# Optimization experiments

Hardware: AMD Instinct MI355X
Metric: run time of the kernel (lower is better)

Reference implementation:

```python
import jax, jax.numpy as jnp
import numpy as np

DIM = 768
CA = 192  # int(dim * mlp_ratio)
T = 8

def setup_inputs() -> dict:
    key = jax.random.key(0)
    ks = jax.random.split(key, 7)
    x = jax.random.normal(ks[0], (197, 128, DIM), dtype=jnp.float32)
    w1 = jax.random.normal(ks[1], (DIM, CA), dtype=jnp.float32) * 0.02
    b1 = jax.random.normal(ks[2], (CA,), dtype=jnp.float32) * 0.02
    conv_w = jax.random.normal(ks[3], (CA, 3), dtype=jnp.float32) * 0.02  # depthwise temporal kernel (3,1,1)
    conv_b = jax.random.normal(ks[4], (CA,), dtype=jnp.float32) * 0.02
    w2 = jax.random.normal(ks[5], (CA, DIM), dtype=jnp.float32) * 0.02
    b2 = jax.random.normal(ks[6], (DIM,), dtype=jnp.float32) * 0.02
    return {"x": x, "w1": w1, "b1": b1, "conv_w": conv_w, "conv_b": conv_b, "w2": w2, "b2": b2}

def reference(x, w1, b1, conv_w, conv_b, w2, b2):
    # x: (L, BT, dim), tokens-first layout (fc1 applied before permute)
    x_id = x
    h = x @ w1 + b1                      # (L, BT, Ca)
    h = jnp.transpose(h, (1, 0, 2))      # (BT, L, Ca)
    BT, L, Ca = h.shape
    B = BT // T
    h = h[:, 1:, :]                      # drop first token (L-1 patch tokens)
    x_cls = h[:, :1, :]                  # (BT, 1, Ca) -- first token AFTER the slice (as in original)
    x_temp = h.reshape(B, T, L - 1, Ca)  # (B, T, P, Ca)
    # Depthwise Conv3d with kernel (3,1,1), pad (1,0,0): pure temporal depthwise conv.
    xp = jnp.pad(x_temp, ((0, 0), (1, 1), (0, 0), (0, 0)))
    x_after = (xp[:, :-2] * conv_w[:, 0] + xp[:, 1:-1] * conv_w[:, 1]
               + xp[:, 2:] * conv_w[:, 2] + conv_b)  # (B, T, P, Ca)
    # Triangular-masked pairwise diff: sum_{i<j} (x_after[j] - x_temp[i]) / 28,
    # computed without materializing the (B,T,T,P,Ca) diff tensor:
    # each x_after[j] appears j times; each x_temp[i] appears (T-1-i) times.
    t = jnp.arange(T, dtype=x.dtype)
    result = (jnp.einsum('t,btpc->bpc', t, x_after)
              - jnp.einsum('t,btpc->bpc', (T - 1) - t, x_temp)) / 28.0
    x_last = (x_temp + result[:, None]).reshape(BT, L - 1, Ca)
    out = jnp.concatenate([x_cls, x_last], axis=1)   # (BT, L, Ca)
    out = jnp.transpose(out, (1, 0, 2))              # (L, BT, Ca)
    out = jax.nn.gelu(out, approximate=False)        # torch nn.GELU default = exact erf
    out = out @ w2 + b2                              # (L, BT, dim)
    return x_id + out
```

## Files before the change

kernel.cpp:

```cpp
#include <hip/hip_runtime.h>
#include <hip/hip_bf16.h>
#include <math.h>

#define DIM   768
#define CA    192
#define NTOK  25216

typedef __attribute__((ext_vector_type(8))) short short8;
typedef __attribute__((ext_vector_type(4))) float f32x4;

static __device__ __forceinline__ short f2bf(float f) {
    union { __hip_bfloat16 b; short s; } u;
    u.b = __float2bfloat16(f);
    return u.s;
}
static __device__ __forceinline__ float gelu_exact(float x) {
    return 0.5f * x * (1.0f + erff(x * 0.70710678118654752440f));
}
static __device__ __forceinline__ void ld16(void* lds, const void* gsrc) {
    __builtin_amdgcn_global_load_lds((const __attribute__((address_space(1))) void*)gsrc,
                                     (__attribute__((address_space(3))) void*)lds, 16, 0, 0);
}

__global__ void prep_kernel(const float* __restrict__ w1, const float* __restrict__ w2,
                            short* __restrict__ w1T, short* __restrict__ w2T) {
    int idx = blockIdx.x * 256 + threadIdx.x;
    if (idx < CA * DIM) {
        int n = idx / DIM, k = idx - n * DIM;
        w1T[idx] = f2bf(w1[k * CA + n]);
        int n2 = idx / CA, k2 = idx - n2 * CA;
        w2T[idx] = f2bf(w2[k2 * DIM + n2]);
    }
}

__global__ __launch_bounds__(256) void gemm1_fused(
        const float* __restrict__ x, const short* __restrict__ w1T,
        const float* __restrict__ b1, const float* __restrict__ conv_w,
        const float* __restrict__ conv_b, short* __restrict__ gq) {
    __shared__ __align__(16) short As[64 * 40];
    __shared__ __align__(16) short Bs[2][96 * 32];

    const int tid = threadIdx.x;
    const int bx  = blockIdx.x;
    const int l   = (bx >> 2) + 1;
    const int hm  = (bx >> 1) & 1;
    const int n0  = (bx & 1) * 96;
    const int R0  = l * 128 + hm * 64;

    const int wave = tid >> 6, lane = tid & 63;
    const int wm = wave >> 1, wn = wave & 1;
    const int lm = lane & 15, lg = lane >> 4;
    const int lk = lg * 8;

    const int arow = tid >> 2;
    const int acol = (tid & 3) * 8;
    const float* xrow = x + (size_t)(R0 + arow) * DIM + acol;

    f32x4 acc[2][3] = {};

    f32x4 av0 = *(const f32x4*)(xrow);
    f32x4 av1 = *(const f32x4*)(xrow + 4);
    if (wave < 3) {
        #pragma unroll
        for (int j = 0; j < 2; j++) {
            int s = (wave * 2 + j) * 64 + lane;
            int m = s >> 2;
            int q = (s & 3) ^ ((m >> 1) & 3);
            ld16(&Bs[0][(wave * 2 + j) * 512], w1T + (size_t)(n0 + m) * DIM + q * 8);
        }
    }

    for (int i = 0; i < 24; i++) {
        const int p = i & 1;
        short8 a8;
        #pragma unroll
        for (int e = 0; e < 4; e++) { a8[e] = f2bf(av0[e]); a8[4 + e] = f2bf(av1[e]); }
        __syncthreads();
        *(short8*)&As[arow * 40 + acol] = a8;
        __syncthreads();
        if (i < 23) {
            const float* xn = xrow + (i + 1) * 32;
            av0 = *(const f32x4*)(xn);
            av1 = *(const f32x4*)(xn + 4);
            if (wave < 3) {
                const int k0n = (i + 1) * 32;
                #pragma unroll
                for (int j = 0; j < 2; j++) {
                    int s = (wave * 2 + j) * 64 + lane;
                    int m = s >> 2;
                    int q = (s & 3) ^ ((m >> 1) & 3);
                    ld16(&Bs[1 - p][(wave * 2 + j) * 512],
                         w1T + (size_t)(n0 + m) * DIM + k0n + q * 8);
                }
            }
        }
        short8 af[2], bf[3];
        af[0] = *(const short8*)&As[(wm * 32 + lm) * 40 + lk];
        af[1] = *(const short8*)&As[(wm * 32 + 16 + lm) * 40 + lk];
        #pragma unroll
        for (int j = 0; j < 3; j++) {
            int rB = wn * 48 + j * 16 + lm;
            int qs = lg ^ ((rB >> 1) & 3);
            bf[j] = *(const short8*)&Bs[p][rB * 32 + qs * 8];
        }
        #pragma unroll
        for (int i2 = 0; i2 < 2; i2++)
            #pragma unroll
            for (int j = 0; j < 3; j++)
                acc[i2][j] = __builtin_amdgcn_mfma_f32_16x16x32_bf16(af[i2], bf[j], acc[i2][j], 0, 0, 0);
    }

    const int g1 = lg & 1;
    #pragma unroll
    for (int j = 0; j < 3; j++) {
        const int c = n0 + wn * 48 + j * 16 + lm;
        const float b1c = b1[c];
        const float cw0 = conv_w[c * 3 + 0];
        const float cw1 = conv_w[c * 3 + 1];
        const float cw2 = conv_w[c * 3 + 2];
        const float cb  = conv_b[c];
        #pragma unroll
        for (int i2 = 0; i2 < 2; i2++) {
            float hv[4];
            #pragma unroll
            for (int r = 0; r < 4; r++) hv[r] = acc[i2][j][r] + b1c;
            float partial = 0.f;
            #pragma unroll
            for (int r = 0; r < 4; r++) {
                const int t = g1 * 4 + r;
                const float tf = (float)t;
                float coef = tf * cw1 - (7.0f - tf);
                if (t <= 6) coef += (tf + 1.0f) * cw0;
                if (t >= 1) coef += (tf - 1.0f) * cw2;
                partial += coef * hv[r];
            }
            const float full = partial + __shfl_xor(partial, 16);
            const float res = cb + full * (1.0f / 28.0f);
            const int row = R0 + wm * 32 + i2 * 16 + lg * 4;
            #pragma unroll
            for (int r = 0; r < 4; r++)
                gq[(size_t)(row + r) * CA + c] = f2bf(gelu_exact(hv[r] + res));
            if (l == 1) {
                const int bt = row - 128;
                #pragma unroll
                for (int r = 0; r < 4; r++)
                    gq[(size_t)(bt + r) * CA + c] = f2bf(gelu_exact(hv[r]));
            }
        }
    }
}

__global__ __launch_bounds__(256) void gemm2_kernel(
        const short* __restrict__ gq, const short* __restrict__ w2T,
        const float* __restrict__ b2, const float* __restrict__ x,
        float* __restrict__ out) {
    __shared__ __align__(16) short As[2][64 * 64];
    __shared__ __align__(16) short Bs[2][128 * 64];

    const int tid = threadIdx.x;
    const int m0 = blockIdx.x * 64;
    const int n0 = blockIdx.y * 128;
    const int wave = tid >> 6, lane = tid & 63;
    const int wm = wave >> 1, wn = wave & 1;
    const int lm = lane & 15, lg = lane >> 4;

    f32x4 acc[2][4] = {};

    #pragma unroll
    for (int j = 0; j < 2; j++) {
        int s = (wave * 2 + j) * 64 + lane;
        int m = s >> 3, q = (s & 7) ^ (m & 7);
        ld16(&As[0][(wave * 2 + j) * 512], gq + (size_t)(m0 + m) * CA + q * 8);
    }
    #pragma unroll
    for (int j = 0; j < 4; j++) {
        int s = (wave * 4 + j) * 64 + lane;
        int m = s >> 3, q = (s & 7) ^ (m & 7);
        ld16(&Bs[0][(wave * 4 + j) * 512], w2T + (size_t)(n0 + m) * CA + q * 8);
    }

    for (int i = 0; i < 3; i++) {
        const int p = i & 1;
        __syncthreads();
        if (i < 2) {
            const int k0 = (i + 1) * 64;
            #pragma unroll
            for (int j = 0; j < 2; j++) {
                int s = (wave * 2 + j) * 64 + lane;
                int m = s >> 3, q = (s & 7) ^ (m & 7);
                ld16(&As[1 - p][(wave * 2 + j) * 512], gq + (size_t)(m0 + m) * CA + k0 + q * 8);
            }
            #pragma unroll
            for (int j = 0; j < 4; j++) {
                int s = (wave * 4 + j) * 64 + lane;
                int m = s >> 3, q = (s & 7) ^ (m & 7);
                ld16(&Bs[1 - p][(wave * 4 + j) * 512], w2T + (size_t)(n0 + m) * CA + k0 + q * 8);
            }
        }
        #pragma unroll
        for (int kk = 0; kk < 2; kk++) {
            const int cb0 = kk * 4 + lg;
            short8 af[2], bf[4];
            #pragma unroll
            for (int i2 = 0; i2 < 2; i2++) {
                int r = wm * 32 + i2 * 16 + lm;
                af[i2] = *(const short8*)&As[p][r * 64 + (cb0 ^ (r & 7)) * 8];
            }
            #pragma unroll
            for (int j = 0; j < 4; j++) {
                int r = wn * 64 + j * 16 + lm;
                bf[j] = *(const short8*)&Bs[p][r * 64 + (cb0 ^ (r & 7)) * 8];
            }
            #pragma unroll
            for (int i2 = 0; i2 < 2; i2++)
                #pragma unroll
                for (int j = 0; j < 4; j++)
                    acc[i2][j] = __builtin_amdgcn_mfma_f32_16x16x32_bf16(af[i2], bf[j], acc[i2][j], 0, 0, 0);
        }
    }

    #pragma unroll
    for (int i2 = 0; i2 < 2; i2++) {
        const int row0 = m0 + wm * 32 + i2 * 16 + lg * 4;
        #pragma unroll
        for (int j = 0; j < 4; j++) {
            const int col = n0 + wn * 64 + j * 16 + lm;
            const float bias = b2[col];
            #pragma unroll
            for (int r = 0; r < 4; r++) {
                const size_t idx = (size_t)(row0 + r) * DIM + col;
                out[idx] = acc[i2][j][r] + x[idx] + bias;
            }
        }
    }
}

extern "C" void kernel_launch(void* const* d_in, const int* in_sizes, int n_in,
                              void* d_out, int out_size, void* d_ws, size_t ws_size,
                              hipStream_t stream) {
    (void)in_sizes; (void)n_in; (void)out_size; (void)ws_size;
    const float* x      = (const float*)d_in[0];
    const float* w1     = (const float*)d_in[1];
    const float* b1     = (const float*)d_in[2];
    const float* conv_w = (const float*)d_in[3];
    const float* conv_b = (const float*)d_in[4];
    const float* w2     = (const float*)d_in[5];
    const float* b2     = (const float*)d_in[6];
    float* out = (float*)d_out;

    char* ws = (char*)d_ws;
    short* g   = (short*)ws;
    short* w1T = (short*)(ws + 9682944);
    short* w2T = (short*)(ws + 9682944 + 294912);

    prep_kernel<<<(CA * DIM + 255) / 256, 256, 0, stream>>>(w1, w2, w1T, w2T);
    gemm1_fused<<<784, 256, 0, stream>>>(x, w1T, b1, conv_w, conv_b, g);
    gemm2_kernel<<<dim3(394, 6), 256, 0, stream>>>(g, w2T, b2, x, out);
}
```

Measured before the change: 195.8 us.

## Drop LDS staging in both GEMMs, load MFMA fragments directly from global

Both GEMM kernels stop using shared memory and barriers. Each wave now loads its bf16/fp32 MFMA operand fragments straight from global memory into registers and double-buffers them there. gemm1 is retiled so each wave owns 16 rows by all 192 output columns, which halves the grid to 392 blocks and removes the cross-wave sync. This trades LDS traffic and __syncthreads for redundant global/L2 reads of the weight matrices across waves and higher register pressure (12 accumulators plus 24 short8 operand buffers).

```diff
diff --git a/kernel.cpp b/kernel.cpp
--- a/kernel.cpp
+++ b/kernel.cpp
@@ -2,9 +2,8 @@
 #include <hip/hip_bf16.h>
 #include <math.h>
 
-#define DIM   768
-#define CA    192
-#define NTOK  25216
+#define DIM 768
+#define CA  192
 
 typedef __attribute__((ext_vector_type(8))) short short8;
 typedef __attribute__((ext_vector_type(4))) float f32x4;
@@ -16,10 +15,6 @@
 }
 static __device__ __forceinline__ float gelu_exact(float x) {
     return 0.5f * x * (1.0f + erff(x * 0.70710678118654752440f));
-}
-static __device__ __forceinline__ void ld16(void* lds, const void* gsrc) {
-    __builtin_amdgcn_global_load_lds((const __attribute__((address_space(1))) void*)gsrc,
-                                     (__attribute__((address_space(3))) void*)lds, 16, 0, 0);
 }
 
 __global__ void prep_kernel(const float* __restrict__ w1, const float* __restrict__ w2,
@@ -37,115 +32,77 @@
         const float* __restrict__ x, const short* __restrict__ w1T,
         const float* __restrict__ b1, const float* __restrict__ conv_w,
         const float* __restrict__ conv_b, short* __restrict__ gq) {
-    __shared__ __align__(16) short As[64 * 40];
-    __shared__ __align__(16) short Bs[2][96 * 32];
+    const int bx   = blockIdx.x;
+    const int l    = (bx >> 1) + 1;
+    const int wave = threadIdx.x >> 6, lane = threadIdx.x & 63;
+    const int R0   = l * 128 + (bx & 1) * 64 + wave * 16;
+    const int lm   = lane & 15, lg = lane >> 4;
 
-    const int tid = threadIdx.x;
-    const int bx  = blockIdx.x;
-    const int l   = (bx >> 2) + 1;
-    const int hm  = (bx >> 1) & 1;
-    const int n0  = (bx & 1) * 96;
-    const int R0  = l * 128 + hm * 64;
+    const float* xA = x   + (size_t)(R0 + lm) * DIM + lg * 8;
+    const short* wB = w1T + (size_t)lm * DIM + lg * 8;
 
-    const int wave = tid >> 6, lane = tid & 63;
-    const int wm = wave >> 1, wn = wave & 1;
-    const int lm = lane & 15, lg = lane >> 4;
-    const int lk = lg * 8;
+    f32x4 acc[12] = {};
 
-    const int arow = tid >> 2;
-    const int acol = (tid & 3) * 8;
-    const float* xrow = x + (size_t)(R0 + arow) * DIM + acol;
+    f32x4 a0 = *(const f32x4*)xA;
+    f32x4 a1 = *(const f32x4*)(xA + 4);
+    short8 bcur[12];
+    #pragma unroll
+    for (int j = 0; j < 12; j++) bcur[j] = *(const short8*)(wB + (size_t)j * 16 * DIM);
 
-    f32x4 acc[2][3] = {};
-
-    f32x4 av0 = *(const f32x4*)(xrow);
-    f32x4 av1 = *(const f32x4*)(xrow + 4);
-    if (wave < 3) {
+    #pragma unroll 2
+    for (int k = 0; k < 24; k++) {
+        f32x4 a0n, a1n;
+        short8 bnxt[12];
+        if (k < 23) {
+            const float* xn = xA + (k + 1) * 32;
+            a0n = *(const f32x4*)xn;
+            a1n = *(const f32x4*)(xn + 4);
+            const short* wn = wB + (k + 1) * 32;
+            #pragma unroll
+            for (int j = 0; j < 12; j++) bnxt[j] = *(const short8*)(wn + (size_t)j * 16 * DIM);
+        }
+        short8 af;
         #pragma unroll
-        for (int j = 0; j < 2; j++) {
-            int s = (wave * 2 + j) * 64 + lane;
-            int m = s >> 2;
-            int q = (s & 3) ^ ((m >> 1) & 3);
-            ld16(&Bs[0][(wave * 2 + j) * 512], w1T + (size_t)(n0 + m) * DIM + q * 8);
-        }
+        for (int e = 0; e < 4; e++) { af[e] = f2bf(a0[e]); af[4 + e] = f2bf(a1[e]); }
+        #pragma unroll
+        for (int j = 0; j < 12; j++)
+            acc[j] = __builtin_amdgcn_mfma_f32_16x16x32_bf16(af, bcur[j], acc[j], 0, 0, 0);
+        a0 = a0n; a1 = a1n;
+        #pragma unroll
+        for (int j = 0; j < 12; j++) bcur[j] = bnxt[j];
     }
 
-    for (int i = 0; i < 24; i++) {
-        const int p = i & 1;
-        short8 a8;
-        #pragma unroll
-        for (int e = 0; e < 4; e++) { a8[e] = f2bf(av0[e]); a8[4 + e] = f2bf(av1[e]); }
-        __syncthreads();
-        *(short8*)&As[arow * 40 + acol] = a8;
-        __syncthreads();
-        if (i < 23) {
-            const float* xn = xrow + (i + 1) * 32;
-            av0 = *(const f32x4*)(xn);
-            av1 = *(const f32x4*)(xn + 4);
-            if (wave < 3) {
-                const int k0n = (i + 1) * 32;
-                #pragma unroll
-                for (int j = 0; j < 2; j++) {
-                    int s = (wave * 2 + j) * 64 + lane;
-                    int m = s >> 2;
-                    int q = (s & 3) ^ ((m >> 1) & 3);
-                    ld16(&Bs[1 - p][(wave * 2 + j) * 512],
-                         w1T + (size_t)(n0 + m) * DIM + k0n + q * 8);
-                }
-            }
-        }
-        short8 af[2], bf[3];
-        af[0] = *(const short8*)&As[(wm * 32 + lm) * 40 + lk];
-        af[1] = *(const short8*)&As[(wm * 32 + 16 + lm) * 40 + lk];
-        #pragma unroll
-        for (int j = 0; j < 3; j++) {
-            int rB = wn * 48 + j * 16 + lm;
-            int qs = lg ^ ((rB >> 1) & 3);
-            bf[j] = *(const short8*)&Bs[p][rB * 32 + qs * 8];
-        }
-        #pragma unroll
-        for (int i2 = 0; i2 < 2; i2++)
-            #pragma unroll
-            for (int j = 0; j < 3; j++)
-                acc[i2][j] = __builtin_amdgcn_mfma_f32_16x16x32_bf16(af[i2], bf[j], acc[i2][j], 0, 0, 0);
-    }
-
-    const int g1 = lg & 1;
+    const int g1  = lg & 1;
+    const int row = R0 + lg * 4;
     #pragma unroll
-    for (int j = 0; j < 3; j++) {
-        const int c = n0 + wn * 48 + j * 16 + lm;
+    for (int j = 0; j < 12; j++) {
+        const int c = j * 16 + lm;
         const float b1c = b1[c];
         const float cw0 = conv_w[c * 3 + 0];
         const float cw1 = conv_w[c * 3 + 1];
         const float cw2 = conv_w[c * 3 + 2];
         const float cb  = conv_b[c];
+        float hv[4];
         #pragma unroll
-        for (int i2 = 0; i2 < 2; i2++) {
-            float hv[4];
-            #pragma unroll
-            for (int r = 0; r < 4; r++) hv[r] = acc[i2][j][r] + b1c;
-            float partial = 0.f;
-            #pragma unroll
-            for (int r = 0; r < 4; r++) {
-                const int t = g1 * 4 + r;
-                const float tf = (float)t;
-                float coef = tf * cw1 - (7.0f - tf);
-                if (t <= 6) coef += (tf + 1.0f) * cw0;
-                if (t >= 1) coef += (tf - 1.0f) * cw2;
-                partial += coef * hv[r];
-            }
-            const float full = partial + __shfl_xor(partial, 16);
-            const float res = cb + full * (1.0f / 28.0f);
-            const int row = R0 + wm * 32 + i2 * 16 + lg * 4;
+        for (int r = 0; r < 4; r++) hv[r] = acc[j][r] + b1c;
+        float partial = 0.f;
+        #pragma unroll
+        for (int r = 0; r < 4; r++) {
+            const int t = g1 * 4 + r;
+            const float tf = (float)t;
+            float coef = tf * cw1 - (7.0f - tf);
+            if (t <= 6) coef += (tf + 1.0f) * cw0;
+            if (t >= 1) coef += (tf - 1.0f) * cw2;
+            partial += coef * hv[r];
+        }
+        const float res = cb + (partial + __shfl_xor(partial, 16)) * (1.0f / 28.0f);
+        #pragma unroll
+        for (int r = 0; r < 4; r++)
+            gq[(size_t)(row + r) * CA + c] = f2bf(gelu_exact(hv[r] + res));
+        if (l == 1) {
             #pragma unroll
             for (int r = 0; r < 4; r++)
-                gq[(size_t)(row + r) * CA + c] = f2bf(gelu_exact(hv[r] + res));
-            if (l == 1) {
-                const int bt = row - 128;
-                #pragma unroll
-                for (int r = 0; r < 4; r++)
-                    gq[(size_t)(bt + r) * CA + c] = f2bf(gelu_exact(hv[r]));
-            }
+                gq[(size_t)(row - 128 + r) * CA + c] = f2bf(gelu_exact(hv[r]));
         }
     }
 }
@@ -154,82 +111,53 @@
         const short* __restrict__ gq, const short* __restrict__ w2T,
         const float* __restrict__ b2, const float* __restrict__ x,
         float* __restrict__ out) {
-    __shared__ __align__(16) short As[2][64 * 64];
-    __shared__ __align__(16) short Bs[2][128 * 64];
+    const int m0 = blockIdx.x * 64, n0 = blockIdx.y * 128;
+    const int wave = threadIdx.x >> 6, lane = threadIdx.x & 63;
+    const int wm = wave & 1, wn = wave >> 1;
+    const int lm = lane & 15, lg = lane >> 4;
+    const int mw = m0 + wm * 32, nw = n0 + wn * 64;
 
-    const int tid = threadIdx.x;
-    const int m0 = blockIdx.x * 64;
-    const int n0 = blockIdx.y * 128;
-    const int wave = tid >> 6, lane = tid & 63;
-    const int wm = wave >> 1, wn = wave & 1;
-    const int lm = lane & 15, lg = lane >> 4;
+    const short* gA  = gq  + (size_t)(mw + lm) * CA + lg * 8;
+    const short* wBp = w2T + (size_t)(nw + lm) * CA + lg * 8;
 
     f32x4 acc[2][4] = {};
+    short8 ac[2], bc[4];
+    #pragma unroll
+    for (int i = 0; i < 2; i++) ac[i] = *(const short8*)(gA + i * 16 * CA);
+    #pragma unroll
+    for (int j = 0; j < 4; j++) bc[j] = *(const short8*)(wBp + j * 16 * CA);
 
     #pragma unroll
-    for (int j = 0; j < 2; j++) {
-        int s = (wave * 2 + j) * 64 + lane;
-        int m = s >> 3, q = (s & 7) ^ (m & 7);
-        ld16(&As[0][(wave * 2 + j) * 512], gq + (size_t)(m0 + m) * CA + q * 8);
-    }
-    #pragma unroll
-    for (int j = 0; j < 4; j++) {
-        int s = (wave * 4 + j) * 64 + lane;
-        int m = s >> 3, q = (s & 7) ^ (m & 7);
-        ld16(&Bs[0][(wave * 4 + j) * 512], w2T + (size_t)(n0 + m) * CA + q * 8);
-    }
-
-    for (int i = 0; i < 3; i++) {
-        const int p = i & 1;
-        __syncthreads();
-        if (i < 2) {
-            const int k0 = (i + 1) * 64;
+    for (int k = 0; k < 6; k++) {
+        short8 an[2], bn[4];
+        if (k < 5) {
             #pragma unroll
-            for (int j = 0; j < 2; j++) {
-                int s = (wave * 2 + j) * 64 + lane;
-                int m = s >> 3, q = (s & 7) ^ (m & 7);
-                ld16(&As[1 - p][(wave * 2 + j) * 512], gq + (size_t)(m0 + m) * CA + k0 + q * 8);
-            }
+            for (int i = 0; i < 2; i++) an[i] = *(const short8*)(gA + i * 16 * CA + (k + 1) * 32);
             #pragma unroll
-            for (int j = 0; j < 4; j++) {
-                int s = (wave * 4 + j) * 64 + lane;
-                int m = s >> 3, q = (s & 7) ^ (m & 7);
-                ld16(&Bs[1 - p][(wave * 4 + j) * 512], w2T + (size_t)(n0 + m) * CA + k0 + q * 8);
-            }
+            for (int j = 0; j < 4; j++) bn[j] = *(const short8*)(wBp + j * 16 * CA + (k + 1) * 32);
         }
         #pragma unroll
-        for (int kk = 0; kk < 2; kk++) {
-            const int cb0 = kk * 4 + lg;
-            short8 af[2], bf[4];
+        for (int i = 0; i < 2; i++)
             #pragma unroll
-            for (int i2 = 0; i2 < 2; i2++) {
-                int r = wm * 32 + i2 * 16 + lm;
-                af[i2] = *(const short8*)&As[p][r * 64 + (cb0 ^ (r & 7)) * 8];
-            }
-            #pragma unroll
-            for (int j = 0; j < 4; j++) {
-                int r = wn * 64 + j * 16 + lm;
-                bf[j] = *(const short8*)&Bs[p][r * 64 + (cb0 ^ (r & 7)) * 8];
-            }
-            #pragma unroll
-            for (int i2 = 0; i2 < 2; i2++)
-                #pragma unroll
-                for (int j = 0; j < 4; j++)
-                    acc[i2][j] = __builtin_amdgcn_mfma_f32_16x16x32_bf16(af[i2], bf[j], acc[i2][j], 0, 0, 0);
-        }
+            for (int j = 0; j < 4; j++)
+                acc[i][j] = __builtin_amdgcn_mfma_f32_16x16x32_bf16(ac[i], bc[j], acc[i][j], 0, 0, 0);
+        #pragma unroll
+        for (int i = 0; i < 2; i++) ac[i] = an[i];
+        #pragma unroll
+        for (int j = 0; j < 4; j++) bc[j] = bn[j];
     }
 
     #pragma unroll
-    for (int i2 = 0; i2 < 2; i2++) {
-        const int row0 = m0 + wm * 32 + i2 * 16 + lg * 4;
+    for (int i = 0; i < 2; i++) {
+        const int row0 = mw + i * 16 + lg * 4;
         #pragma unroll
         for (int j = 0; j < 4; j++) {
-            const int col = n0 + wn * 64 + j * 16 + lm;
+            const int col = nw + j * 16 + lm;
             const float bias = b2[col];
             #pragma unroll
             for (int r = 0; r < 4; r++) {
                 const size_t idx = (size_t)(row0 + r) * DIM + col;
-                out[idx] = acc[i2][j][r] + x[idx] + bias;
+                out[idx] = acc[i][j][r] + x[idx] + bias;
             }
         }
     }
@@ -254,6 +182,6 @@
     short* w2T = (short*)(ws + 9682944 + 294912);
 
     prep_kernel<<<(CA * DIM + 255) / 256, 256, 0, stream>>>(w1, w2, w1T, w2T);
-    gemm1_fused<<<784, 256, 0, stream>>>(x, w1T, b1, conv_w, conv_b, g);
+    gemm1_fused<<<392, 256, 0, stream>>>(x, w1T, b1, conv_w, conv_b, g);
     gemm2_kernel<<<dim3(394, 6), 256, 0, stream>>>(g, w2T, b2, x, out);
 }
```

After: 263.1 us. 34.4% more time.
